# Kernel optimization log

Measured on AMD Instinct MI355X. Metric: run time of the kernel, lower is better.

Reference implementation:

```python
import jax, jax.numpy as jnp
import numpy as np
from jax import lax

ALPHA = 2.0       # spikingjelly ATan surrogate default alpha
NUM_HEADS = 8
V_TH = 1.0

@jax.custom_vjp
def spike(x):
    return (x >= 0.0).astype(x.dtype)

def _spike_fwd(x):
    return spike(x), x

def _spike_bwd(x, g):
    # ATan surrogate: alpha/2 / (1 + (pi/2 * alpha * x)^2)
    return (g * (ALPHA / 2.0) / (1.0 + (jnp.pi / 2.0 * ALPHA * x) ** 2),)

spike.defvjp(_spike_fwd, _spike_bwd)

def lif(x, w):
    # ParametricLIFNode, step_mode='m', decay_input=True, hard reset to 0,
    # detach_reset=True. x: [T, ...]; w: learned scalar, decay = sigmoid(w).
    decay = jax.nn.sigmoid(w)
    def step(v, xt):
        v = v + (xt - v) * decay
        s = spike(v - V_TH)
        v = v * (1.0 - lax.stop_gradient(s))  # detach_reset hard reset
        return v, s
    _, s = lax.scan(step, jnp.zeros_like(x[0]), x)
    return s

def layernorm(x, g, b, eps=1e-5):
    m = x.mean(-1, keepdims=True)
    var = ((x - m) ** 2).mean(-1, keepdims=True)
    return (x - m) / jnp.sqrt(var + eps) * g + b

def setup_inputs() -> dict:
    key = jax.random.key(0)
    ks = jax.random.split(key, 16)
    T, B, C, H, W = 4, 16, 512, 16, 16
    hidden = 4 * C
    s = 0.02
    inp = {
        'x': jax.random.normal(ks[0], (T, B, C, H, W), jnp.float32),
        'conv_w': jax.random.normal(ks[1], (C, 1, 3, 3), jnp.float32) * s,
        'conv_b': jnp.zeros((C,), jnp.float32),
        'ln1_g': jnp.ones((C,), jnp.float32),
        'ln1_b': jnp.zeros((C,), jnp.float32),
        'qkv_w': jax.random.normal(ks[2], (3 * C, C), jnp.float32) * s,
        'proj_w': jax.random.normal(ks[3], (C, C), jnp.float32) * s,
        'proj_b': jnp.zeros((C,), jnp.float32),
        'ln2_g': jnp.ones((C,), jnp.float32),
        'ln2_b': jnp.zeros((C,), jnp.float32),
        'fc1_w': jax.random.normal(ks[4], (hidden, C), jnp.float32) * s,
        'fc1_b': jnp.zeros((hidden,), jnp.float32),
        'fc2_w': jax.random.normal(ks[5], (C, hidden), jnp.float32) * s,
        'fc2_b': jnp.zeros((C,), jnp.float32),
        'lif_w': jnp.zeros((8,), jnp.float32),  # init_tau=2 -> w=0
    }
    return inp

def reference(x, conv_w, conv_b, ln1_g, ln1_b, qkv_w, proj_w, proj_b,
              ln2_g, ln2_b, fc1_w, fc1_b, fc2_w, fc2_b, lif_w):
    T, B, C, H, W = x.shape
    N = H * W
    nH = NUM_HEADS
    d = C // nH
    scale = d ** -0.5

    # conv positional embedding on spikes, residual
    s = lif(x, lif_w[0])
    sf = s.reshape(T * B, C, H, W)
    pos = lax.conv_general_dilated(
        sf, conv_w, (1, 1), 'SAME', feature_group_count=C,
        dimension_numbers=('NCHW', 'OIHW', 'NCHW'))
    pos = pos + conv_b[None, :, None, None]
    x = x + pos.reshape(T, B, C, H, W)

    # tokens: [T, B, N, C]
    xt = x.reshape(T, B, C, N).transpose(0, 1, 3, 2)

    # spiking linear attention
    h = lif(layernorm(xt, ln1_g, ln1_b), lif_w[1])
    qkv = h @ qkv_w.T                              # [T,B,N,3C]
    qkv = qkv.reshape(T, B, N, 3, nH, d).transpose(3, 0, 1, 4, 2, 5)  # [3,T,B,h,N,d]
    q = lif(qkv[0], lif_w[2])
    k = lif(qkv[1], lif_w[3])
    v = lif(qkv[2], lif_w[4])
    kv = jnp.einsum('tbhnd,tbhne->tbhde', k, v)    # [T,B,h,d,d]
    a = jnp.einsum('tbhnd,tbhde->tbhne', q, kv) * scale
    a = a.transpose(0, 1, 3, 2, 4).reshape(T, B, N, C)
    a = lif(a, lif_w[5])
    a = a @ proj_w.T + proj_b
    xt = xt + a

    # spiking MLP
    h = lif(layernorm(xt, ln2_g, ln2_b), lif_w[6])
    h = h @ fc1_w.T + fc1_b
    h = lif(h, lif_w[7])
    h = h @ fc2_w.T + fc2_b
    xt = xt + h

    return xt.transpose(0, 1, 3, 2).reshape(T, B, C, H, W)
```

## Files before the change

kernel.cpp:

```cpp
#include <hip/hip_runtime.h>

typedef unsigned long long u64;
typedef unsigned int u32;
typedef float  floatx4 __attribute__((ext_vector_type(4)));
typedef short  short8  __attribute__((ext_vector_type(8)));

#define T_ 4

static __device__ __forceinline__ float b2f(unsigned short u){
  union { unsigned int i; float f; } x; x.i = ((unsigned int)u) << 16; return x.f;
}
static __device__ __forceinline__ unsigned short f2b(float f){
  unsigned int u = __float_as_uint(f);
  unsigned int r = (u + 0x7FFFu + ((u >> 16) & 1u)) >> 16;
  return (unsigned short)r;
}
static __device__ __forceinline__ float sigmoidf_(float x){ return 1.f / (1.f + expf(-x)); }

static __device__ __forceinline__ void gll16(const void* g, void* l){
  __builtin_amdgcn_global_load_lds(
      (const __attribute__((address_space(1))) void*)g,
      (__attribute__((address_space(3))) void*)l, 16, 0, 0);
}

__global__ __launch_bounds__(256) void wsplit_kernel(const float* __restrict__ qkvw,
    const float* __restrict__ projw, const float* __restrict__ fc1w,
    const float* __restrict__ fc2w, unsigned short* __restrict__ hi,
    unsigned short* __restrict__ lo){
  int i = blockIdx.x * 256 + threadIdx.x;
  const float* src; int off;
  if (i < 786432)      { src = qkvw; off = i; }
  else if (i < 1048576){ src = projw; off = i - 786432; }
  else if (i < 2097152){ src = fc1w;  off = i - 1048576; }
  else                 { src = fc2w;  off = i - 2097152; }
  float f = src[off];
  unsigned short h = f2b(f);
  float r = f - b2f(h);
  hi[i] = h; lo[i] = f2b(r);
}

__global__ __launch_bounds__(256) void conv_lif_kernel(const float* __restrict__ x,
    const float* __restrict__ cw, const float* __restrict__ cb,
    const float* __restrict__ lifw, float* __restrict__ xt){
  __shared__ __align__(16) float xs[16 * 260];
  __shared__ u64 sbits[16][5];
  int bb = blockIdx.x & 15, cg = blockIdx.x >> 4;
  int c0 = cg * 16;
  int tid = threadIdx.x;
  int lane = tid & 63, w = tid >> 6;
  int cl = tid & 15;
  float D = sigmoidf_(lifw[0]);
  float cwv[9];
  #pragma unroll
  for (int j = 0; j < 9; ++j) cwv[j] = cw[(c0 + cl) * 9 + j];
  float cbv = cb[c0 + cl];
  float v[16];
  #pragma unroll
  for (int k = 0; k < 16; ++k) v[k] = 0.f;

  for (int t = 0; t < T_; ++t){
    #pragma unroll
    for (int j = 0; j < 4; ++j){
      int kk = __builtin_amdgcn_readfirstlane(w + 4 * j);
      const float* grow = x + (((size_t)t * 16 + bb) * 512 + c0 + kk) * 256 + lane * 4;
      gll16(grow, &xs[kk * 260]);
    }
    __syncthreads();
    #pragma unroll
    for (int k = 0; k < 16; ++k){
      float xv = xs[k * 260 + tid];
      v[k] = v[k] + (xv - v[k]) * D;
      bool sp = v[k] >= 1.f;
      u64 bal = __ballot(sp);
      if (lane == 0) sbits[k][w] = bal;
      v[k] = sp ? 0.f : v[k];
    }
    __syncthreads();
    u64 sw0 = sbits[cl][0], sw1 = sbits[cl][1], sw2 = sbits[cl][2], sw3 = sbits[cl][3];
    #pragma unroll
    for (int i = 0; i < 16; ++i){
      int n = (tid >> 4) + 16 * i;
      int hh = n >> 4, ww = n & 15;
      float acc = cbv;
      #pragma unroll
      for (int dy = -1; dy <= 1; ++dy){
        int yy = hh + dy; if ((unsigned)yy >= 16u) continue;
        #pragma unroll
        for (int dx = -1; dx <= 1; ++dx){
          int xx = ww + dx; if ((unsigned)xx >= 16u) continue;
          int p = yy * 16 + xx;
          u64 word = (p < 64) ? sw0 : (p < 128) ? sw1 : (p < 192) ? sw2 : sw3;
          if ((word >> (p & 63)) & 1ull) acc += cwv[(dy + 1) * 3 + (dx + 1)];
        }
      }
      float xv = xs[cl * 260 + n];
      xt[(((size_t)t * 16 + bb) * 256 + n) * 512 + c0 + cl] = xv + acc;
    }
    __syncthreads();
  }
}

__global__ __launch_bounds__(256) void ln_lif_kernel(const float* __restrict__ xt,
    const float* __restrict__ g, const float* __restrict__ be,
    const float* __restrict__ lifw, int lidx, u64* __restrict__ obits){
  int bn = blockIdx.x; int tid = threadIdx.x;
  int lane = tid & 63, wid = tid >> 6;
  int c0 = tid, c1 = tid + 256;
  __shared__ float ps[8];
  float D = sigmoidf_(lifw[lidx]);
  float g0 = g[c0], g1 = g[c1];
  float b0 = be[c0], b1 = be[c1];
  float v0 = 0.f, v1 = 0.f;
  for (int t = 0; t < T_; ++t){
    size_t base = ((size_t)t * 4096 + bn) * 512;
    float x0 = xt[base + c0], x1 = xt[base + c1];
    float s = x0 + x1, q = x0 * x0 + x1 * x1;
    #pragma unroll
    for (int m = 32; m > 0; m >>= 1){
      s += __shfl_xor(s, m, 64);
      q += __shfl_xor(q, m, 64);
    }
    if (lane == 0){ ps[wid * 2] = s; ps[wid * 2 + 1] = q; }
    __syncthreads();
    float S = ps[0] + ps[2] + ps[4] + ps[6];
    float Q = ps[1] + ps[3] + ps[5] + ps[7];
    __syncthreads();
    float mean = S * (1.f / 512.f);
    float var = Q * (1.f / 512.f) - mean * mean;
    float inv = 1.f / sqrtf(var + 1e-5f);
    float y0 = (x0 - mean) * inv * g0 + b0;
    float y1 = (x1 - mean) * inv * g1 + b1;
    v0 = v0 + (y0 - v0) * D; bool s0 = v0 >= 1.f;
    v1 = v1 + (y1 - v1) * D; bool s1 = v1 >= 1.f;
    u64 bal0 = __ballot(s0);
    u64 bal1 = __ballot(s1);
    if (lane == 0){
      size_t rb = ((size_t)t * 4096 + bn) * 8;
      obits[rb + wid] = bal0;
      obits[rb + 4 + wid] = bal1;
    }
    v0 = s0 ? 0.f : v0; v1 = s1 ? 0.f : v1;
  }
}

__global__ __launch_bounds__(256) void lif_bits_kernel(const float* __restrict__ in,
    u64* __restrict__ bits, const float* __restrict__ lifw, int lidx){
  int tid = blockIdx.x * 256 + threadIdx.x;
  int j = tid & 511; int bn = tid >> 9;
  float D = sigmoidf_(lifw[lidx]);
  float v = 0.f;
  #pragma unroll
  for (int t = 0; t < T_; ++t){
    int m = t * 4096 + bn;
    float xv = in[(size_t)m * 512 + j];
    v = v + (xv - v) * D;
    bool sp = v >= 1.f;
    u64 bal = __ballot(sp);
    if ((threadIdx.x & 63) == 0) bits[(size_t)m * 8 + (j >> 6)] = bal;
    v = sp ? 0.f : v;
  }
}

__global__ __launch_bounds__(256) void gemm_fused(
    const u64* __restrict__ Abits, int ars,
    const unsigned short* __restrict__ Whi, const unsigned short* __restrict__ Wlo, int ldw,
    const float* __restrict__ bias,
    float* __restrict__ xtio, float* __restrict__ outF,
    u64* __restrict__ outBits,
    int K, int mode, const float* __restrict__ lifw, int lidx){
  extern __shared__ __align__(16) char smemraw[];
  unsigned short* Bh = (unsigned short*)smemraw;
  unsigned short* Bl = (unsigned short*)(smemraw + 16384);
  u32* Alds = (u32*)(smemraw + 32768);
  u64* tab  = (u64*)(smemraw + 40960);
  int bn0 = blockIdx.x * 32;
  int n0  = blockIdx.y * 128;
  int tid = threadIdx.x, lane = tid & 63, wid = tid >> 6;
  int wn = wid * 32;
  int lm = lane & 15, quad = lane >> 4;
  int qs = quad * 8;
  int r4 = lane >> 2;
  int swz = ((lane & 3) ^ ((lane >> 3) & 3)) * 8;
  int rB0 = wid * 16 + r4, rB1 = rB0 + 64;
  const unsigned short* ph0 = Whi + (size_t)(n0 + rB0) * ldw + swz;
  const unsigned short* ph1 = Whi + (size_t)(n0 + rB1) * ldw + swz;
  const unsigned short* pl0 = Wlo + (size_t)(n0 + rB0) * ldw + swz;
  const unsigned short* pl1 = Wlo + (size_t)(n0 + rB1) * ldw + swz;
  int lofs = __builtin_amdgcn_readfirstlane(wid * 512);
  int sx = (quad ^ ((lm >> 1) & 3)) << 3;

  auto stageA = [&](int w0){
    #pragma unroll
    for (int i = 0; i < 4; ++i){
      int idx = tid + i * 256;
      int r = idx & 127, w64 = idx >> 7;
      size_t g = (size_t)((r >> 5) * 4096 + bn0 + (r & 31));
      u64 vb = Abits[g * ars + w0 + w64];
      Alds[(2 * w64) * 128 + r]     = (u32)vb;
      Alds[(2 * w64 + 1) * 128 + r] = (u32)(vb >> 32);
    }
  };
  auto stageB = [&](int buf, int kb){
    int bo = buf << 12;
    gll16(ph0 + kb, Bh + bo + lofs);
    gll16(ph1 + kb, Bh + bo + 2048 + lofs);
    gll16(pl0 + kb, Bl + bo + lofs);
    gll16(pl1 + kb, Bl + bo + 2048 + lofs);
  };

  if (tid < 16){
    u64 e = 0;
    #pragma unroll
    for (int j = 0; j < 4; ++j) if ((tid >> j) & 1) e |= 0x3F80ull << (16 * j);
    tab[tid] = e;
  }
  stageA(0);
  stageB(0, 0);
  __syncthreads();

  floatx4 acc[8][2];
  #pragma unroll
  for (int i = 0; i < 8; ++i)
    #pragma unroll
    for (int j = 0; j < 2; ++j){ acc[i][j][0]=0.f; acc[i][j][1]=0.f; acc[i][j][2]=0.f; acc[i][j][3]=0.f; }

  int cur = 0;
  for (int kb = 0; kb < K; kb += 32){
    if (kb && (kb & 511) == 0){
      stageA(kb >> 6);
      __syncthreads();
    }
    if (kb + 32 < K) stageB(cur ^ 1, kb + 32);
    int bo = cur << 12;
    int wl = (kb >> 5) & 15;
    short8 bh[2], bl[2];
    #pragma unroll
    for (int in = 0; in < 2; ++in){
      bh[in] = *(const short8*)(&Bh[bo + (wn + in * 16 + lm) * 32 + sx]);
      bl[in] = *(const short8*)(&Bl[bo + (wn + in * 16 + lm) * 32 + sx]);
    }
    __builtin_amdgcn_s_setprio(1);
    #pragma unroll
    for (int im = 0; im < 8; ++im){
      u32 wv = Alds[wl * 128 + im * 16 + lm];
      u32 by = wv >> qs;
      union { u64 d[2]; short8 s; } c;
      c.d[0] = tab[by & 15u];
      c.d[1] = tab[(by >> 4) & 15u];
      acc[im][0] = __builtin_amdgcn_mfma_f32_16x16x32_bf16(c.s, bh[0], acc[im][0], 0, 0, 0);
      acc[im][1] = __builtin_amdgcn_mfma_f32_16x16x32_bf16(c.s, bh[1], acc[im][1], 0, 0, 0);
      acc[im][0] = __builtin_amdgcn_mfma_f32_16x16x32_bf16(c.s, bl[0], acc[im][0], 0, 0, 0);
      acc[im][1] = __builtin_amdgcn_mfma_f32_16x16x32_bf16(c.s, bl[1], acc[im][1], 0, 0, 0);
    }
    __builtin_amdgcn_s_setprio(0);
    __syncthreads();
    cur ^= 1;
  }

  if (mode == 0 || mode == 3){
    #pragma unroll
    for (int im = 0; im < 8; ++im){
      int row0 = im * 16 + quad * 4;
      #pragma unroll
      for (int in = 0; in < 2; ++in){
        int col = n0 + wn + in * 16 + lm;
        float bv = bias ? bias[col] : 0.f;
        #pragma unroll
        for (int r = 0; r < 4; ++r){
          int row = row0 + r;
          int t = row >> 5; int bq = bn0 + (row & 31);
          size_t gg = (size_t)t * 4096 + bq;
          float vv = acc[im][in][r] + bv + xtio[gg * 512 + col];
          if (mode == 0){
            xtio[gg * 512 + col] = vv;
          } else {
            outF[(((size_t)t * 16 + (bq >> 8)) * 512 + col) * 256 + (bq & 255)] = vv;
          }
        }
      }
    }
    return;
  }

  u32* bits32 = (u32*)(smemraw + 32768);
  u64* ob; int obrs, obwb;
  if (mode == 1){ ob = outBits + (size_t)(n0 >> 9) * 131072; obrs = 8; obwb = (n0 & 511) >> 6; }
  else          { ob = outBits; obrs = 32; obwb = n0 >> 6; }
  float D = sigmoidf_(lifw[mode == 1 ? (2 + (n0 >> 9)) : lidx]);
  float bv0 = bias ? bias[n0 + wn + lm] : 0.f;
  float bv1 = bias ? bias[n0 + wn + 16 + lm] : 0.f;
  #pragma unroll
  for (int r = 0; r < 4; ++r){
    float vA0 = 0.f, vA1 = 0.f, vB0 = 0.f, vB1 = 0.f;
    #pragma unroll
    for (int t = 0; t < 4; ++t){
      float pA0 = acc[2*t][0][r] + bv0;   vA0 += (pA0 - vA0) * D; bool sA0 = vA0 >= 1.f; vA0 = sA0 ? 0.f : vA0;
      float pA1 = acc[2*t][1][r] + bv1;   vA1 += (pA1 - vA1) * D; bool sA1 = vA1 >= 1.f; vA1 = sA1 ? 0.f : vA1;
      float pB0 = acc[2*t+1][0][r] + bv0; vB0 += (pB0 - vB0) * D; bool sB0 = vB0 >= 1.f; vB0 = sB0 ? 0.f : vB0;
      float pB1 = acc[2*t+1][1][r] + bv1; vB1 += (pB1 - vB1) * D; bool sB1 = vB1 >= 1.f; vB1 = sB1 ? 0.f : vB1;
      u64 balA0 = __ballot(sA0), balA1 = __ballot(sA1);
      u64 balB0 = __ballot(sB0), balB1 = __ballot(sB1);
      if (lane < 4){
        int q = lane;
        u32 wA = (u32)((balA0 >> (16*q)) & 0xFFFFull) | ((u32)((balA1 >> (16*q)) & 0xFFFFull) << 16);
        u32 wB = (u32)((balB0 >> (16*q)) & 0xFFFFull) | ((u32)((balB1 >> (16*q)) & 0xFFFFull) << 16);
        bits32[(t * 32 + q * 4 + r) * 4 + wid]      = wA;
        bits32[(t * 32 + 16 + q * 4 + r) * 4 + wid] = wB;
      }
    }
  }
  __syncthreads();
  {
    int t = tid >> 6, bnl = (tid >> 1) & 31, j = tid & 1;
    size_t g = (size_t)t * 4096 + bn0 + bnl;
    int idx = (t * 32 + bnl) * 4 + 2 * j;
    u64 wv = (u64)bits32[idx] | ((u64)bits32[idx + 1] << 32);
    ob[g * obrs + obwb + j] = wv;
  }
}

__global__ __launch_bounds__(256) void attn_a_kernel(const u64* __restrict__ bits,
    float* __restrict__ aout){
  int tbh = blockIdx.x;
  int h = tbh & 7, b = (tbh >> 3) & 15, t = tbh >> 7;
  int m0 = t * 4096 + b * 256;
  int tid = threadIdx.x, lane = tid & 63, wid = tid >> 6;
  __shared__ u64 QW[256], KW[256], VW[256];
  __shared__ u64 kbt[64][4], vbt[64][4];
  __shared__ __align__(16) unsigned short Bs[64 * 72];
  {
    size_t base = (size_t)(m0 + tid) * 8 + h;
    QW[tid] = bits[base];
    KW[tid] = bits[131072 + base];
    VW[tid] = bits[262144 + base];
  }
  __syncthreads();
  {
    int i = tid & 63, w = tid >> 6;
    const u64* kwp = &KW[w * 64];
    const u64* vwp = &VW[w * 64];
    u64 bk = 0, bv = 0;
    for (int nn = 0; nn < 64; ++nn){
      bk |= ((kwp[nn] >> i) & 1ull) << nn;
      bv |= ((vwp[nn] >> i) & 1ull) << nn;
    }
    kbt[i][w] = bk; vbt[i][w] = bv;
  }
  __syncthreads();
  #pragma unroll
  for (int e = 0; e < 16; ++e){
    int idx = tid * 16 + e;
    int i = idx >> 6, j = idx & 63;
    int cnt = __popcll(kbt[i][0] & vbt[j][0]) + __popcll(kbt[i][1] & vbt[j][1])
            + __popcll(kbt[i][2] & vbt[j][2]) + __popcll(kbt[i][3] & vbt[j][3]);
    Bs[j * 72 + i] = f2b((float)cnt);
  }
  __syncthreads();
  int lm = lane & 15, quad = lane >> 4;
  int wm = wid * 64;
  u64 qw[4];
  #pragma unroll
  for (int im = 0; im < 4; ++im) qw[im] = QW[wm + im * 16 + lm];
  floatx4 acc[4][4];
  #pragma unroll
  for (int i = 0; i < 4; ++i)
    #pragma unroll
    for (int j = 0; j < 4; ++j){ acc[i][j][0]=0.f; acc[i][j][1]=0.f; acc[i][j][2]=0.f; acc[i][j][3]=0.f; }
  #pragma unroll
  for (int kb = 0; kb < 64; kb += 32){
    short8 af[4], bf[4];
    #pragma unroll
    for (int im = 0; im < 4; ++im){
      u32 byte = (u32)(qw[im] >> (kb + quad * 8)) & 0xFFu;
      union { u32 u[4]; short8 s; } c;
      c.u[0] = ((byte & 1u)        | ((byte & 2u) << 15))        * 0x3F80u;
      c.u[1] = (((byte >> 2) & 1u) | (((byte >> 3) & 1u) << 16)) * 0x3F80u;
      c.u[2] = (((byte >> 4) & 1u) | (((byte >> 5) & 1u) << 16)) * 0x3F80u;
      c.u[3] = (((byte >> 6) & 1u) | (((byte >> 7) & 1u) << 16)) * 0x3F80u;
      af[im] = c.s;
    }
    #pragma unroll
    for (int in = 0; in < 4; ++in)
      bf[in] = *(const short8*)(&Bs[(in * 16 + lm) * 72 + kb + quad * 8]);
    #pragma unroll
    for (int im = 0; im < 4; ++im)
      #pragma unroll
      for (int in = 0; in < 4; ++in)
        acc[im][in] = __builtin_amdgcn_mfma_f32_16x16x32_bf16(af[im], bf[in], acc[im][in], 0, 0, 0);
  }
  float* ob = aout + (size_t)m0 * 512 + h * 64;
  #pragma unroll
  for (int im = 0; im < 4; ++im){
    int nr0 = wm + im * 16 + quad * 4;
    #pragma unroll
    for (int in = 0; in < 4; ++in){
      int j = in * 16 + lm;
      #pragma unroll
      for (int r = 0; r < 4; ++r)
        ob[(size_t)(nr0 + r) * 512 + j] = acc[im][in][r] * 0.125f;
    }
  }
}

extern "C" void kernel_launch(void* const* d_in, const int* in_sizes, int n_in,
                              void* d_out, int out_size, void* d_ws, size_t ws_size,
                              hipStream_t stream){
  const float* x     = (const float*)d_in[0];
  const float* convw = (const float*)d_in[1];
  const float* convb = (const float*)d_in[2];
  const float* ln1g  = (const float*)d_in[3];
  const float* ln1b  = (const float*)d_in[4];
  const float* qkvw  = (const float*)d_in[5];
  const float* projw = (const float*)d_in[6];
  const float* projb = (const float*)d_in[7];
  const float* ln2g  = (const float*)d_in[8];
  const float* ln2b  = (const float*)d_in[9];
  const float* fc1w  = (const float*)d_in[10];
  const float* fc1b  = (const float*)d_in[11];
  const float* fc2w  = (const float*)d_in[12];
  const float* fc2b  = (const float*)d_in[13];
  const float* lifw  = (const float*)d_in[14];
  float* outp = (float*)d_out;

  char* wsb = (char*)d_ws;
  float* XT           = (float*)wsb;
  float* AF32         = (float*)(wsb + 33554432);
  unsigned short* WHI = (unsigned short*)(wsb + 67108864);
  unsigned short* WLO = (unsigned short*)(wsb + 73400320);
  u64* QBITS          = (u64*)(wsb + 79691776);
  u64* H12            = (u64*)(wsb + 82837504);
  u64* ASB            = (u64*)(wsb + 83886080);
  u64* HBITS          = (u64*)(wsb + 84934656);
  const int OFF_QKV = 0, OFF_PROJ = 786432, OFF_FC1 = 1048576, OFF_FC2 = 2097152;
  const int GEMM_LDS = 41088;

  wsplit_kernel<<<12288, 256, 0, stream>>>(qkvw, projw, fc1w, fc2w, WHI, WLO);
  conv_lif_kernel<<<512, 256, 0, stream>>>(x, convw, convb, lifw, XT);
  ln_lif_kernel<<<4096, 256, 0, stream>>>(XT, ln1g, ln1b, lifw, 1, H12);
  gemm_fused<<<dim3(128, 12), 256, GEMM_LDS, stream>>>(H12, 8,
      WHI + OFF_QKV, WLO + OFF_QKV, 512, nullptr,
      nullptr, nullptr, QBITS, 512, 1, lifw, 0);
  attn_a_kernel<<<512, 256, 0, stream>>>(QBITS, AF32);
  lif_bits_kernel<<<8192, 256, 0, stream>>>(AF32, ASB, lifw, 5);
  gemm_fused<<<dim3(128, 4), 256, GEMM_LDS, stream>>>(ASB, 8,
      WHI + OFF_PROJ, WLO + OFF_PROJ, 512, projb,
      XT, nullptr, nullptr, 512, 0, lifw, 0);
  ln_lif_kernel<<<4096, 256, 0, stream>>>(XT, ln2g, ln2b, lifw, 6, H12);
  gemm_fused<<<dim3(128, 16), 256, GEMM_LDS, stream>>>(H12, 8,
      WHI + OFF_FC1, WLO + OFF_FC1, 512, fc1b,
      nullptr, nullptr, HBITS, 512, 2, lifw, 7);
  gemm_fused<<<dim3(128, 4), 256, GEMM_LDS, stream>>>(HBITS, 32,
      WHI + OFF_FC2, WLO + OFF_FC2, 2048, fc2b,
      XT, outp, nullptr, 2048, 3, lifw, 0);
}
```

Before: 409.2 us.

## Give each wave private B tiles and drop per-k-step block barrier

Each wave now loads only the weight rows it consumes into its own region of LDS, so the block-wide __syncthreads after every k-step is replaced by per-wave s_waitcnt on vmcnt. The prefetch is moved two stages ahead: two buffers are primed before the loop and the next load is issued after the MFMAs. This is meant to remove barrier stalls and let waves drift independently. It adds a barrier before re-staging A and before the epilogue reuses LDS. It relies on global_load_lds completion ordering via vmcnt, and the stageA global loads also count toward vmcnt.

```diff
diff --git a/kernel.cpp b/kernel.cpp
--- a/kernel.cpp
+++ b/kernel.cpp
@@ -179,14 +179,13 @@
   int wn = wid * 32;
   int lm = lane & 15, quad = lane >> 4;
   int qs = quad * 8;
-  int r4 = lane >> 2;
   int swz = ((lane & 3) ^ ((lane >> 3) & 3)) * 8;
-  int rB0 = wid * 16 + r4, rB1 = rB0 + 64;
-  const unsigned short* ph0 = Whi + (size_t)(n0 + rB0) * ldw + swz;
-  const unsigned short* ph1 = Whi + (size_t)(n0 + rB1) * ldw + swz;
-  const unsigned short* pl0 = Wlo + (size_t)(n0 + rB0) * ldw + swz;
-  const unsigned short* pl1 = Wlo + (size_t)(n0 + rB1) * ldw + swz;
-  int lofs = __builtin_amdgcn_readfirstlane(wid * 512);
+  int rW = wn + (lane >> 2);
+  const unsigned short* pH0 = Whi + (size_t)(n0 + rW) * ldw + swz;
+  const unsigned short* pH1 = pH0 + (size_t)16 * ldw;
+  const unsigned short* pL0 = Wlo + (size_t)(n0 + rW) * ldw + swz;
+  const unsigned short* pL1 = pL0 + (size_t)16 * ldw;
+  int b0 = __builtin_amdgcn_readfirstlane(wid << 10);
   int sx = (quad ^ ((lm >> 1) & 3)) << 3;
 
   auto stageA = [&](int w0){
@@ -201,11 +200,11 @@
     }
   };
   auto stageB = [&](int buf, int kb){
-    int bo = buf << 12;
-    gll16(ph0 + kb, Bh + bo + lofs);
-    gll16(ph1 + kb, Bh + bo + 2048 + lofs);
-    gll16(pl0 + kb, Bl + bo + lofs);
-    gll16(pl1 + kb, Bl + bo + 2048 + lofs);
+    int bo = (buf << 12) + b0;
+    gll16(pH0 + kb, Bh + bo);
+    gll16(pH1 + kb, Bh + bo + 512);
+    gll16(pL0 + kb, Bl + bo);
+    gll16(pL1 + kb, Bl + bo + 512);
   };
 
   if (tid < 16){
@@ -216,6 +215,7 @@
   }
   stageA(0);
   stageB(0, 0);
+  stageB(1, 32);
   __syncthreads();
 
   floatx4 acc[8][2];
@@ -227,10 +227,13 @@
   int cur = 0;
   for (int kb = 0; kb < K; kb += 32){
     if (kb && (kb & 511) == 0){
+      __syncthreads();
       stageA(kb >> 6);
       __syncthreads();
     }
-    if (kb + 32 < K) stageB(cur ^ 1, kb + 32);
+    if (kb + 32 < K) asm volatile("s_waitcnt vmcnt(4)" ::: "memory");
+    else             asm volatile("s_waitcnt vmcnt(0)" ::: "memory");
+    __builtin_amdgcn_sched_barrier(0);
     int bo = cur << 12;
     int wl = (kb >> 5) & 15;
     short8 bh[2], bl[2];
@@ -253,7 +256,8 @@
       acc[im][1] = __builtin_amdgcn_mfma_f32_16x16x32_bf16(c.s, bl[1], acc[im][1], 0, 0, 0);
     }
     __builtin_amdgcn_s_setprio(0);
-    __syncthreads();
+    __builtin_amdgcn_sched_barrier(0);
+    if (kb + 64 < K) stageB(cur, kb + 64);
     cur ^= 1;
   }
 
@@ -282,6 +286,7 @@
     return;
   }
 
+  __syncthreads();
   u32* bits32 = (u32*)(smemraw + 32768);
   u64* ob; int obrs, obwb;
   if (mode == 1){ ob = outBits + (size_t)(n0 >> 9) * 131072; obrs = 8; obwb = (n0 & 511) >> 6; }
```

Measured after the change: 396.8 us. 3.0% less time.
